# Kernel optimization log

Measured on AMD Instinct MI355X. Metric: run time of the kernel, lower is better.

Reference implementation:

```python
import jax, jax.numpy as jnp
import numpy as np

TEMPERATURE = 0.07
BASE_TEMPERATURE = 0.07
NUM_HEADS = 4


def setup_inputs() -> dict:
    key = jax.random.key(0)
    k1, k2 = jax.random.split(key)
    features = jax.random.normal(k1, (2048, 2, 256), dtype=jnp.float32)
    labels = jax.random.randint(k2, (2048, 10), 0, 2).astype(jnp.float32)
    return {"features": features, "labels": labels}


def reference(features, labels):
    B, V, E = features.shape
    H = NUM_HEADS
    fs = E // H
    N = B * V

    # torch.cat(torch.unbind(features, dim=1), dim=0): view-major stacking
    f = jnp.transpose(features, (1, 0, 2)).reshape(N, H, fs)
    # F.normalize(dim=-1) with eps=1e-12 clamp
    norm = jnp.sqrt(jnp.sum(f * f, axis=-1, keepdims=True))
    f = f / jnp.maximum(norm, 1e-12)

    # per-head pairwise similarities: dot[i, j, h] = <f[i,h], f[j,h]>  (N, N, H)
    dot = jnp.einsum('ihf,jhf->ijh', f, f)
    heads = jnp.argmax(dot, axis=-1)              # (N, N) head chosen per (anchor, positive)
    dotT = dot / TEMPERATURE

    # logits_max is over j for fixed (i, head); detached in the original
    maxh = jax.lax.stop_gradient(jnp.max(dotT, axis=1))   # (N, H)

    # positive mask, tiled across views, self removed
    mask = (labels @ labels.T) > 0                # (B, B) bool
    mask = jnp.tile(mask, (V, V)).astype(f.dtype)  # (N, N)
    logits_mask = 1.0 - jnp.eye(N, dtype=f.dtype)  # (N, N)
    mask = mask * logits_mask

    # masked exp-sum per (anchor, head): S[i,h] = sum_j lm[i,j] * exp(dotT[i,j,h] - maxh[i,h])
    exp_l = jnp.exp(dotT - maxh[:, None, :])       # (N, N, H)
    S = jnp.einsum('ij,ijh->ih', logits_mask, exp_l)  # (N, H)
    logS = jnp.log(S)

    # select per-pair head: log_prob[i,k] = dotT[i,k,h(i,k)] - maxh[i,h(i,k)] - logS[i,h(i,k)]
    dot_sel = jnp.take_along_axis(dotT, heads[..., None], axis=2)[..., 0]  # (N, N)
    max_sel = jnp.take_along_axis(maxh, heads, axis=1)                     # (N, N)
    logS_sel = jnp.take_along_axis(logS, heads, axis=1)                    # (N, N)
    log_prob = dot_sel - max_sel - logS_sel

    mean_log_prob_pos = jnp.sum(mask * log_prob, axis=1) / jnp.sum(mask, axis=1)
    loss = -(TEMPERATURE / BASE_TEMPERATURE) * mean_log_prob_pos

    finite = jnp.isfinite(loss)
    return jnp.sum(jnp.where(finite, loss, 0.0)) / jnp.sum(finite)
```

## Files before the change

### kernel.cpp

```cpp
#include <hip/hip_runtime.h>
#include <math.h>

#define BS    2048
#define NROW  4096
#define EDIM  256
#define INVT  (1.0f/0.07f)

typedef float  float4v __attribute__((ext_vector_type(4)));
typedef short  short8v __attribute__((ext_vector_type(8)));

static __device__ __forceinline__ unsigned short f2bf(float x) {
    unsigned u = __builtin_bit_cast(unsigned, x);
    u += 0x7fffu + ((u >> 16) & 1u);
    return (unsigned short)(u >> 16);
}

static __device__ __forceinline__ void gload_lds16(const void* g, void* l) {
    __builtin_amdgcn_global_load_lds(
        (const __attribute__((address_space(1))) unsigned int*)g,
        (__attribute__((address_space(3))) unsigned int*)l, 16, 0, 0);
}

__global__ void prep_kernel(const float* __restrict__ feat, const float* __restrict__ labels,
                            unsigned short* __restrict__ fnb, unsigned* __restrict__ bits,
                            float* __restrict__ zacc) {
    const int b = blockIdx.x, t = threadIdx.x;
    if (b < NROW) {
        int bb = b & (BS - 1);
        int v = b >> 11;
        float x = feat[(size_t)bb * (2 * EDIM) + (size_t)v * EDIM + t];
        float ss = x * x;
#pragma unroll
        for (int off = 32; off > 0; off >>= 1)
            ss += __shfl_xor(ss, off, 64);
        float nrm = fmaxf(sqrtf(ss), 1e-12f);
        fnb[(size_t)b * EDIM + t] = f2bf(x / nrm);
    } else {
        int g = (b - NROW) * 256 + t;
        unsigned bb = 0;
#pragma unroll
        for (int d = 0; d < 10; ++d)
            bb |= (labels[g * 10 + d] != 0.0f ? 1u : 0u) << d;
        bits[g] = bb;
        for (int k = g; k < NROW * 9 + 3; k += 2048) zacc[k] = 0.0f;
    }
}

__global__ __launch_bounds__(256, 4) void main_kernel(
    const unsigned short* __restrict__ fnb, const unsigned* __restrict__ bits,
    float* __restrict__ S, float* __restrict__ Num, float* __restrict__ Cnt) {

    __shared__ unsigned short shB[2][32 * 256];

    const int tid  = threadIdx.x;
    const int lane = tid & 63;
    const int wave = tid >> 6;
    const int quad = lane >> 4;
    const int ml   = lane & 15;
    const int xr   = ml & 7;
    const int i0   = blockIdx.x * 64 + wave * 16;
    const int jc0  = blockIdx.y * 256;

    short8v af[4][2];
    {
        const unsigned short* ap = fnb + (size_t)(i0 + ml) * EDIM + quad * 8;
#pragma unroll
        for (int h = 0; h < 4; ++h)
#pragma unroll
            for (int kk = 0; kk < 2; ++kk)
                af[h][kk] = *(const short8v*)(ap + h * 64 + kk * 32);
    }

    unsigned ibr[4];
#pragma unroll
    for (int r = 0; r < 4; ++r)
        ibr[r] = bits[(i0 + quad * 4 + r) & (BS - 1)];

    float    Sp[4][4] = {};
    float    np[4] = {};
    unsigned cpk[4] = {};

    auto STAGE = [&](int st, int buf) {
#pragma unroll
        for (int q = 0; q < 4; ++q) {
            const int G   = tid + 256 * q;
            const int row = G >> 5;
            const int gg  = (G & 31) ^ (row & 7);
            gload_lds16(fnb + (size_t)(jc0 + st * 32 + row) * EDIM + gg * 8,
                        &shB[buf][G * 8]);
        }
    };

    STAGE(0, 0);
    __syncthreads();

    for (int st = 0; st < 8; ++st) {
        const int cur = st & 1;
        if (st < 7) STAGE(st + 1, cur ^ 1);
        const int j0 = jc0 + st * 32;

#pragma unroll
        for (int js = 0; js < 2; ++js) {
            const unsigned jb = bits[(j0 + js * 16 + ml) & (BS - 1)];

            float4v dacc[4];
#pragma unroll
            for (int h = 0; h < 4; ++h) dacc[h] = (float4v){0.f, 0.f, 0.f, 0.f};
#pragma unroll
            for (int h = 0; h < 4; ++h)
#pragma unroll
                for (int kk = 0; kk < 2; ++kk) {
                    const int gsw = ((h * 8 + kk * 4 + quad) ^ xr) * 8;
                    short8v bf = *(const short8v*)(&shB[cur][(js * 16 + ml) * 256 + gsw]);
                    dacc[h] = __builtin_amdgcn_mfma_f32_16x16x32_bf16(af[h][kk], bf, dacc[h], 0, 0, 0);
                }

            const int j = j0 + js * 16 + ml;
#pragma unroll
            for (int r = 0; r < 4; ++r) {
                const int i = i0 + quad * 4 + r;
                const float d0 = dacc[0][r];
                const float d1 = dacc[1][r];
                const float d2 = dacc[2][r];
                const float d3 = dacc[3][r];
                float bd = d0; int bh = 0;
                if (d1 > bd) { bd = d1; bh = 1; }
                if (d2 > bd) { bd = d2; bh = 2; }
                if (d3 > bd) { bd = d3; bh = 3; }
                const bool off = (i != j);
                const float e0 = __expf(fmaf(d0, INVT, -INVT));
                const float e1 = __expf(fmaf(d1, INVT, -INVT));
                const float e2 = __expf(fmaf(d2, INVT, -INVT));
                const float e3 = __expf(fmaf(d3, INVT, -INVT));
                if (off) {
                    Sp[r][0] += e0; Sp[r][1] += e1; Sp[r][2] += e2; Sp[r][3] += e3;
                }
                if (off && (ibr[r] & jb)) {
                    np[r] += bd;
                    cpk[r] += 1u << (bh * 8);
                }
            }
        }
        __syncthreads();
    }

#pragma unroll
    for (int r = 0; r < 4; ++r) {
        const int i = i0 + quad * 4 + r;
        float v[9];
        v[0] = np[r];
#pragma unroll
        for (int h = 0; h < 4; ++h) v[1 + h] = Sp[r][h];
#pragma unroll
        for (int h = 0; h < 4; ++h) v[5 + h] = (float)((cpk[r] >> (8 * h)) & 255u);
#pragma unroll
        for (int k = 0; k < 9; ++k) {
            float x = v[k];
            x += __shfl_xor(x, 1, 64);
            x += __shfl_xor(x, 2, 64);
            x += __shfl_xor(x, 4, 64);
            x += __shfl_xor(x, 8, 64);
            v[k] = x;
        }
        if (ml == 0) {
            atomicAdd(&Num[i], v[0] * INVT);
#pragma unroll
            for (int h = 0; h < 4; ++h) atomicAdd(&S[i * 4 + h], v[1 + h]);
#pragma unroll
            for (int h = 0; h < 4; ++h) atomicAdd(&Cnt[i * 4 + h], v[5 + h]);
        }
    }
}

__global__ void final_kernel(const float* __restrict__ S, const float* __restrict__ Num,
                             const float* __restrict__ Cnt, float* __restrict__ red,
                             unsigned* __restrict__ done, float* __restrict__ out) {
    const int tid = threadIdx.x;
    const int i = blockIdx.x * 256 + tid;
    float c = 0.f;
    float numr = Num[i];
#pragma unroll
    for (int h = 0; h < 4; ++h) {
        float sh = S[i * 4 + h];
        float ch = Cnt[i * 4 + h];
        numr -= ch * (INVT + logf(sh));
        c += ch;
    }
    float ls = 0.f, lc = 0.f;
    if (c > 0.f) { ls = -(numr / c); lc = 1.f; }

    __shared__ float rs[256], rc[256];
    rs[tid] = ls; rc[tid] = lc;
    __syncthreads();
    for (int s = 128; s > 0; s >>= 1) {
        if (tid < s) { rs[tid] += rs[tid + s]; rc[tid] += rc[tid + s]; }
        __syncthreads();
    }
    if (tid == 0) {
        atomicAdd(&red[0], rs[0]);
        atomicAdd(&red[1], rc[0]);
        __threadfence();
        if (atomicAdd(done, 1u) == 15u) {
            float s = atomicAdd(&red[0], 0.0f);
            float cc = atomicAdd(&red[1], 0.0f);
            out[0] = s / cc;
        }
    }
}

extern "C" void kernel_launch(void* const* d_in, const int* in_sizes, int n_in,
                              void* d_out, int out_size, void* d_ws, size_t ws_size,
                              hipStream_t stream) {
    const float* feat = (const float*)d_in[0];
    const float* labels = (const float*)d_in[1];
    float* out = (float*)d_out;

    char* ws = (char*)d_ws;
    unsigned short* fnb = (unsigned short*)ws;
    float* S = (float*)(ws + (size_t)NROW * EDIM * sizeof(unsigned short));
    float* Num = S + NROW * 4;
    float* Cnt = Num + NROW;
    float* red = Cnt + NROW * 4;
    unsigned* done = (unsigned*)(red + 2);
    unsigned* bits = done + 1;

    prep_kernel<<<NROW + 8, 256, 0, stream>>>(feat, labels, fnb, bits, S);
    main_kernel<<<dim3(64, 16), 256, 0, stream>>>(fnb, bits, S, Num, Cnt);
    final_kernel<<<16, 256, 0, stream>>>(S, Num, Cnt, red, done, out);
}
```

Before: 109.4 us.

## Exploit similarity symmetry by computing only lower-triangular tiles

Since the per-head dot products are symmetric, the grid now covers only block tiles on or below the diagonal (544 instead of 1024 blocks). Each block keeps only j<i entries and credits them to both the row and the column: column partial sums of exp values, selected dot and head counts are gathered in shared memory and then added atomically to the global accumulators. The aim is to roughly halve the MFMA and exp work, at the cost of extra shuffles, shared-memory atomics and global atomics, plus an uneven per-block workload.

```diff
diff --git a/kernel.cpp b/kernel.cpp
--- a/kernel.cpp
+++ b/kernel.cpp
@@ -51,6 +51,8 @@
     float* __restrict__ S, float* __restrict__ Num, float* __restrict__ Cnt) {
 
     __shared__ unsigned short shB[2][32 * 256];
+    __shared__ float    colS[256 * 5];
+    __shared__ unsigned colC[256];
 
     const int tid  = threadIdx.x;
     const int lane = tid & 63;
@@ -58,8 +60,16 @@
     const int quad = lane >> 4;
     const int ml   = lane & 15;
     const int xr   = ml & 7;
-    const int i0   = blockIdx.x * 64 + wave * 16;
-    const int jc0  = blockIdx.y * 256;
+
+    int idr = blockIdx.x, by = 0;
+    while (idr >= 64 - 4 * by) { idr -= 64 - 4 * by; ++by; }
+    const int bx  = 4 * by + idr;
+    const int i0  = bx * 64 + wave * 16;
+    const int jc0 = by * 256;
+
+#pragma unroll
+    for (int k = 0; k < 5; ++k) colS[tid + 256 * k] = 0.0f;
+    colC[tid] = 0u;
 
     short8v af[4][2];
     {
@@ -116,6 +126,8 @@
                 }
 
             const int j = j0 + js * 16 + ml;
+            float cS0 = 0.f, cS1 = 0.f, cS2 = 0.f, cS3 = 0.f, cNp = 0.f;
+            unsigned cCt = 0u;
 #pragma unroll
             for (int r = 0; r < 4; ++r) {
                 const int i = i0 + quad * 4 + r;
@@ -127,18 +139,37 @@
                 if (d1 > bd) { bd = d1; bh = 1; }
                 if (d2 > bd) { bd = d2; bh = 2; }
                 if (d3 > bd) { bd = d3; bh = 3; }
-                const bool off = (i != j);
+                const bool keep = (j < i);
                 const float e0 = __expf(fmaf(d0, INVT, -INVT));
                 const float e1 = __expf(fmaf(d1, INVT, -INVT));
                 const float e2 = __expf(fmaf(d2, INVT, -INVT));
                 const float e3 = __expf(fmaf(d3, INVT, -INVT));
-                if (off) {
+                if (keep) {
                     Sp[r][0] += e0; Sp[r][1] += e1; Sp[r][2] += e2; Sp[r][3] += e3;
-                }
-                if (off && (ibr[r] & jb)) {
-                    np[r] += bd;
+                    cS0 += e0; cS1 += e1; cS2 += e2; cS3 += e3;
+                }
+                if (keep && (ibr[r] & jb)) {
+                    np[r] += bd;  cNp += bd;
                     cpk[r] += 1u << (bh * 8);
-                }
+                    cCt    += 1u << (bh * 8);
+                }
+            }
+            cS0 += __shfl_xor(cS0, 16, 64); cS0 += __shfl_xor(cS0, 32, 64);
+            cS1 += __shfl_xor(cS1, 16, 64); cS1 += __shfl_xor(cS1, 32, 64);
+            cS2 += __shfl_xor(cS2, 16, 64); cS2 += __shfl_xor(cS2, 32, 64);
+            cS3 += __shfl_xor(cS3, 16, 64); cS3 += __shfl_xor(cS3, 32, 64);
+            cNp += __shfl_xor(cNp, 16, 64); cNp += __shfl_xor(cNp, 32, 64);
+            cCt += __shfl_xor(cCt, 16, 64); cCt += __shfl_xor(cCt, 32, 64);
+            if (quad == 0) {
+                const int jj = st * 32 + js * 16 + ml;
+                if (cS0 != 0.f) {
+                    atomicAdd(&colS[jj * 5 + 0], cS0);
+                    atomicAdd(&colS[jj * 5 + 1], cS1);
+                    atomicAdd(&colS[jj * 5 + 2], cS2);
+                    atomicAdd(&colS[jj * 5 + 3], cS3);
+                    atomicAdd(&colS[jj * 5 + 4], cNp);
+                }
+                if (cCt) atomicAdd(&colC[jj], cCt);
             }
         }
         __syncthreads();
@@ -168,6 +199,26 @@
             for (int h = 0; h < 4; ++h) atomicAdd(&S[i * 4 + h], v[1 + h]);
 #pragma unroll
             for (int h = 0; h < 4; ++h) atomicAdd(&Cnt[i * 4 + h], v[5 + h]);
+        }
+    }
+
+    __syncthreads();
+    {
+        const int j = tid;
+        const float s0 = colS[j * 5 + 0];
+        if (s0 != 0.f) {
+            const int gj = jc0 + j;
+            atomicAdd(&S[gj * 4 + 0], s0);
+            atomicAdd(&S[gj * 4 + 1], colS[j * 5 + 1]);
+            atomicAdd(&S[gj * 4 + 2], colS[j * 5 + 2]);
+            atomicAdd(&S[gj * 4 + 3], colS[j * 5 + 3]);
+            atomicAdd(&Num[gj], colS[j * 5 + 4] * INVT);
+            const unsigned ct = colC[j];
+            if (ct) {
+#pragma unroll
+                for (int h = 0; h < 4; ++h)
+                    atomicAdd(&Cnt[gj * 4 + h], (float)((ct >> (8 * h)) & 255u));
+            }
         }
     }
 }
@@ -225,6 +276,6 @@
     unsigned* bits = done + 1;
 
     prep_kernel<<<NROW + 8, 256, 0, stream>>>(feat, labels, fnb, bits, S);
-    main_kernel<<<dim3(64, 16), 256, 0, stream>>>(fnb, bits, S, Num, Cnt);
+    main_kernel<<<544, 256, 0, stream>>>(fnb, bits, S, Num, Cnt);
     final_kernel<<<16, 256, 0, stream>>>(S, Num, Cnt, red, done, out);
 }
```

Result: slower. 140.0 us (+28.0%).
